# Kernel tuning notes

Measured on AMD Instinct MI355X. Metric: run time of the kernel, lower is better.

The kernel has to match this reference:

```python
import jax, jax.numpy as jnp
import numpy as np

B, S, D = 32, 2048, 1024
TEMP = 9.0  # RelaxedBernoulli temperature (torch.tensor([9]))


def setup_inputs() -> dict:
    key = jax.random.key(0)
    ks = jax.random.split(key, 12)
    sd = 1.0 / np.sqrt(D)
    sd2 = 1.0 / np.sqrt(2 * D)
    return {
        "h_t": jax.random.normal(ks[0], (B, D), jnp.float32),
        "h_s": jax.random.normal(ks[1], (B, S, D), jnp.float32),
        "auxi_hs": jax.random.normal(ks[2], (B, S, D), jnp.float32),
        "noise_u": jax.random.uniform(ks[3], (B, S, 1), jnp.float32),
        # linear_map: Linear(2*dim, 1) with bias
        "Wmap": jax.random.normal(ks[4], (2 * D,), jnp.float32) * sd2,
        "bmap": jax.random.normal(ks[5], (), jnp.float32) * sd2,
        # mlp_h: Linear(dim, dim) + Tanh + Linear(dim, 1)
        "W1": jax.random.normal(ks[6], (D, D), jnp.float32) * sd,
        "b1": jax.random.normal(ks[7], (D,), jnp.float32) * sd,
        "W2": jax.random.normal(ks[8], (D,), jnp.float32) * sd,
        "b2": jax.random.normal(ks[9], (), jnp.float32) * sd,
        # linear_out: Linear(2*dim, dim, bias=False) (attn_type='dot')
        "Wout": jax.random.normal(ks[10], (D, 2 * D), jnp.float32) * sd2,
    }


def reference(h_t, h_s, auxi_hs, noise_u, Wmap, bmap, W1, b1, W2, b2, Wout):
    # h_t: (B, D) one-step query; h_s, auxi_hs: (B, S, D)
    d = h_s.shape[-1]
    # linear_map(concat(auxi_hs, H_t)) without materializing the (B,S,2D) concat
    Wm_a, Wm_t = Wmap[:d], Wmap[d:]
    logits_p = jnp.einsum('bsd,d->bs', auxi_hs, Wm_a) + (h_t @ Wm_t)[:, None] + bmap  # (B,S)
    logits_p = logits_p[..., None]  # (B,S,1); note logit(sigmoid(x)) == x
    # RelaxedBernoulli(temp=9, probs=sigmoid(logits_p)).sample() with explicit uniform noise
    eps = 1e-7
    u = jnp.clip(noise_u, eps, 1.0 - eps)
    logistic = jnp.log(u) - jnp.log1p(-u)  # (B,S,1)
    G = jax.nn.sigmoid((logits_p + logistic) / TEMP)  # (B,S,1)
    # mlp_h(h_s): Linear -> tanh -> Linear
    e = jnp.einsum('bsd,d->bs', jnp.tanh(jnp.einsum('bsd,ed->bse', h_s, W1) + b1), W2) + b2
    e = e[..., None]  # (B,S,1)
    # custom softmax: max over dim 0 (batch!), exp, gate
    v = jnp.max(e, axis=0, keepdims=True)  # (1,S,1)
    scores = jnp.exp(e - v) * G  # (B,S,1)
    align = scores[..., 0] / jnp.sum(scores[..., 0], axis=1, keepdims=True)  # (B,S)
    c = jnp.einsum('bs,bsd->bd', align, h_s)  # (B,D)
    attn_h = jnp.tanh(jnp.concatenate([c, h_t], axis=-1) @ Wout.T)  # (B,D)
    return attn_h, align
```

## Files before the change

kernel.cpp:

```cpp
#include <hip/hip_runtime.h>
#include <hip/hip_bf16.h>
#include <math.h>

#define B_ 32
#define S_ 2048
#define D_ 1024
#define TEMP_ 9.0f

typedef __attribute__((ext_vector_type(8))) short short8;
typedef __attribute__((ext_vector_type(4))) float f32x4;
typedef __attribute__((ext_vector_type(4))) unsigned short ushort4v;

__device__ __forceinline__ unsigned short f2b(float f) {
  union { float f; unsigned int u; } v; v.f = f;
  unsigned int r = v.u;
  r += 0x7fffu + ((r >> 16) & 1u);
  return (unsigned short)(r >> 16);
}
__device__ __forceinline__ float b2f(unsigned short b) {
  union { float f; unsigned int u; } v; v.u = ((unsigned int)b) << 16;
  return v.f;
}
__device__ __forceinline__ float tanh_fast(float x) {
  float ez = __expf(2.f * x);
  return 1.f - __fdividef(2.f, ez + 1.f);
}

#define GLOAD_LDS16(g, l) \
  __builtin_amdgcn_global_load_lds((const __attribute__((address_space(1))) void*)(g), \
                                   (__attribute__((address_space(3))) void*)(l), 16, 0, 0)

__global__ void k_conv(const float* __restrict__ src, unsigned short* __restrict__ dst, int n8) {
  int i = blockIdx.x * 256 + threadIdx.x;
  if (i >= n8) return;
  const float4* g = reinterpret_cast<const float4*>(src) + (size_t)i * 2;
  float4 x0 = g[0], x1 = g[1];
  uint4 w;
  w.x = f2b(x0.x) | ((unsigned)f2b(x0.y) << 16);
  w.y = f2b(x0.z) | ((unsigned)f2b(x0.w) << 16);
  w.z = f2b(x1.x) | ((unsigned)f2b(x1.y) << 16);
  w.w = f2b(x1.z) | ((unsigned)f2b(x1.w) << 16);
  reinterpret_cast<uint4*>(dst)[i] = w;
}

__global__ void k0_tdot(const float* __restrict__ h_t, const float* __restrict__ Wmap,
                        const float* __restrict__ bmap, float* __restrict__ tdot) {
  int b = blockIdx.x;
  int t = threadIdx.x;
  float p = 0.f;
  for (int k = t; k < D_; k += 256) p += h_t[b*D_ + k] * Wmap[D_ + k];
  __shared__ float red[256];
  red[t] = p; __syncthreads();
  for (int off = 128; off > 0; off >>= 1) { if (t < off) red[t] += red[t+off]; __syncthreads(); }
  if (t == 0) tdot[b] = red[0] + bmap[0];
}

__global__ void k1_gate(const float* __restrict__ aux, const float* __restrict__ Wmap,
                        const float* __restrict__ noise, const float* __restrict__ tdot,
                        float* __restrict__ Gout) {
  int w = (blockIdx.x * 256 + threadIdx.x) >> 6;
  int lane = threadIdx.x & 63;
  const float4* arow = reinterpret_cast<const float4*>(aux + (size_t)w * D_);
  const float4* wrow = reinterpret_cast<const float4*>(Wmap);
  float p = 0.f;
  for (int it = 0; it < 4; ++it) {
    float4 a = arow[it*64 + lane];
    float4 m = wrow[it*64 + lane];
    p += a.x*m.x + a.y*m.y + a.z*m.z + a.w*m.w;
  }
  for (int msk = 32; msk > 0; msk >>= 1) p += __shfl_xor(p, msk);
  if (lane == 0) {
    int b = w >> 11;
    float logits = p + tdot[b];
    float u = noise[w];
    u = fminf(fmaxf(u, 1e-7f), 1.f - 1e-7f);
    float logistic = logf(u) - log1pf(-u);
    float x = (logits + logistic) / TEMP_;
    Gout[w] = 1.f / (1.f + expf(-x));
  }
}

#define BK3 32
#define NT3 (D_ / BK3)

extern __shared__ unsigned short lds2[];

__global__ __launch_bounds__(512, 2) void k2_pipe(
    const unsigned short* __restrict__ Ag, const unsigned short* __restrict__ Bg,
    const float* __restrict__ b1, const float* __restrict__ W2,
    float* __restrict__ e_buf) {
  int hw = blockIdx.x;
  int xcd = hw & 7;
  int sub = hw >> 3;
  int cc  = sub & 3;
  int rc  = xcd + 8 * (sub >> 2);
  int rowBase = rc * 256;
  int colBase = cc * 256;

  int t = threadIdx.x;
  int lane = t & 63;
  int wv = t >> 6;
  int wr = wv >> 2, wc = wv & 3;
  int kslot = lane >> 4;

  int aOff[8], bOff[4];
#pragma unroll
  for (int m = 0; m < 8; ++m) {
    int ra = wr * 128 + m * 16 + (lane & 15);
    aOff[m] = ra * 64 + ((kslot ^ ((ra >> 1) & 3)) << 4);
  }
#pragma unroll
  for (int n = 0; n < 4; ++n) {
    int rb = wc * 64 + n * 16 + (lane & 15);
    bOff[n] = 16384 + rb * 64 + ((kslot ^ ((rb >> 1) & 3)) << 4);
  }

  const unsigned short* gA[2];
  const unsigned short* gB[2];
  int dstOff[2];
#pragma unroll
  for (int i = 0; i < 2; ++i) {
    int c = i * 512 + t;
    int r = c >> 2;
    int clog = (c & 3) ^ ((r >> 1) & 3);
    gA[i] = Ag + (size_t)(rowBase + r) * D_ + clog * 8;
    gB[i] = Bg + (size_t)(colBase + r) * D_ + clog * 8;
    dstOff[i] = c * 16;
  }

  f32x4 acc[8][4] = {};

#define STAGE(TT) do {                                                         \
    char* _ba = (char*)lds2 + ((TT) & 3) * 32768;                              \
    GLOAD_LDS16(gA[0] + (TT) * 32, _ba + dstOff[0]);                           \
    GLOAD_LDS16(gA[1] + (TT) * 32, _ba + dstOff[1]);                           \
    GLOAD_LDS16(gB[0] + (TT) * 32, _ba + 16384 + dstOff[0]);                   \
    GLOAD_LDS16(gB[1] + (TT) * 32, _ba + 16384 + dstOff[1]);                   \
  } while (0)

#define K2_TILE(T, VM, DO_STAGE) do {                                          \
    asm volatile("s_waitcnt lgkmcnt(0)\n\ts_waitcnt vmcnt(" #VM ")" ::: "memory"); \
    __builtin_amdgcn_s_barrier();                                              \
    if (DO_STAGE) STAGE((T) + 3);                                              \
    const char* _ab = (const char*)lds2 + ((T) & 3) * 32768;                   \
    short8 af[8], bf[4];                                                       \
    _Pragma("unroll")                                                          \
    for (int n = 0; n < 4; ++n)                                                \
      bf[n] = *reinterpret_cast<const short8*>(_ab + bOff[n]);                 \
    _Pragma("unroll")                                                          \
    for (int m = 0; m < 4; ++m)                                                \
      af[m] = *reinterpret_cast<const short8*>(_ab + aOff[m]);                 \
    __builtin_amdgcn_s_setprio(1);                                             \
    _Pragma("unroll")                                                          \
    for (int m = 0; m < 4; ++m)                                                \
      _Pragma("unroll")                                                        \
      for (int n = 0; n < 4; ++n)                                              \
        acc[m][n] = __builtin_amdgcn_mfma_f32_16x16x32_bf16(af[m], bf[n], acc[m][n], 0, 0, 0); \
    _Pragma("unroll")                                                          \
    for (int m = 4; m < 8; ++m)                                                \
      af[m] = *reinterpret_cast<const short8*>(_ab + aOff[m]);                 \
    _Pragma("unroll")                                                          \
    for (int m = 4; m < 8; ++m)                                                \
      _Pragma("unroll")                                                        \
      for (int n = 0; n < 4; ++n)                                              \
        acc[m][n] = __builtin_amdgcn_mfma_f32_16x16x32_bf16(af[m], bf[n], acc[m][n], 0, 0, 0); \
    __builtin_amdgcn_s_setprio(0);                                             \
  } while (0)

  STAGE(0); STAGE(1); STAGE(2);
#pragma unroll
  for (int tt = 0; tt < 28; ++tt) K2_TILE(tt, 8, true);
  K2_TILE(28, 8, true);
  K2_TILE(29, 8, false);
  K2_TILE(30, 4, false);
  K2_TILE(31, 0, false);
#undef K2_TILE
#undef STAGE

  float b1v[4], w2v[4];
#pragma unroll
  for (int n = 0; n < 4; ++n) {
    int col = colBase + wc * 64 + n * 16 + (lane & 15);
    b1v[n] = b1[col];
    w2v[n] = W2[col];
  }
#pragma unroll
  for (int m = 0; m < 8; ++m) {
#pragma unroll
    for (int j = 0; j < 4; ++j) {
      float s = 0.f;
#pragma unroll
      for (int n = 0; n < 4; ++n)
        s += tanh_fast(acc[m][n][j] + b1v[n]) * w2v[n];
      s += __shfl_xor(s, 1);
      s += __shfl_xor(s, 2);
      s += __shfl_xor(s, 4);
      s += __shfl_xor(s, 8);
      if ((lane & 15) == 0) {
        int row = rowBase + wr * 128 + m * 16 + ((lane >> 4) << 2) + j;
        atomicAdd(&e_buf[row], s);
      }
    }
  }
}

#define BM 128
#define BN 128
#define BK 64
__global__ __launch_bounds__(256) void k2_egemm_f32(
    const float* __restrict__ h_s, const float* __restrict__ W1,
    const float* __restrict__ b1, const float* __restrict__ W2,
    float* __restrict__ e_buf) {
  __shared__ unsigned short As[BM * BK];
  __shared__ unsigned short Bs[BN * BK];
  int bid = blockIdx.x;
  int colBase = (bid & 7) * BN;
  int rowBase = (bid >> 3) * BM;
  int t = threadIdx.x;
  int lane = t & 63;
  int wave = t >> 6;
  int wr = wave >> 1, wc = wave & 1;
  f32x4 acc[4][4] = {};
  for (int k0 = 0; k0 < D_; k0 += BK) {
    __syncthreads();
    for (int i = 0; i < 4; ++i) {
      int flat = i*256 + t;
      int r = flat >> 3;
      int c8 = flat & 7;
      int byte = (r*128 + c8*16) ^ ((r & 7) << 4);
      {
        const float4* g = reinterpret_cast<const float4*>(h_s + (size_t)(rowBase + r)*D_ + k0 + c8*8);
        float4 x0 = g[0], x1 = g[1];
        uint4 w;
        w.x = f2b(x0.x) | ((unsigned)f2b(x0.y) << 16);
        w.y = f2b(x0.z) | ((unsigned)f2b(x0.w) << 16);
        w.z = f2b(x1.x) | ((unsigned)f2b(x1.y) << 16);
        w.w = f2b(x1.z) | ((unsigned)f2b(x1.w) << 16);
        *reinterpret_cast<uint4*>(reinterpret_cast<char*>(As) + byte) = w;
      }
      {
        const float4* g = reinterpret_cast<const float4*>(W1 + (size_t)(colBase + r)*D_ + k0 + c8*8);
        float4 x0 = g[0], x1 = g[1];
        uint4 w;
        w.x = f2b(x0.x) | ((unsigned)f2b(x0.y) << 16);
        w.y = f2b(x0.z) | ((unsigned)f2b(x0.w) << 16);
        w.z = f2b(x1.x) | ((unsigned)f2b(x1.y) << 16);
        w.w = f2b(x1.z) | ((unsigned)f2b(x1.w) << 16);
        *reinterpret_cast<uint4*>(reinterpret_cast<char*>(Bs) + byte) = w;
      }
    }
    __syncthreads();
    for (int kk = 0; kk < BK; kk += 32) {
      short8 af[4], bf[4];
      int kByte = kk*2 + ((lane >> 4) << 4);
      for (int m = 0; m < 4; ++m) {
        int r = wr*64 + m*16 + (lane & 15);
        int byte = (r*128 + kByte) ^ ((r & 7) << 4);
        af[m] = *reinterpret_cast<const short8*>(reinterpret_cast<const char*>(As) + byte);
      }
      for (int n = 0; n < 4; ++n) {
        int r = wc*64 + n*16 + (lane & 15);
        int byte = (r*128 + kByte) ^ ((r & 7) << 4);
        bf[n] = *reinterpret_cast<const short8*>(reinterpret_cast<const char*>(Bs) + byte);
      }
      for (int m = 0; m < 4; ++m)
        for (int n = 0; n < 4; ++n)
          acc[m][n] = __builtin_amdgcn_mfma_f32_16x16x32_bf16(af[m], bf[n], acc[m][n], 0, 0, 0);
    }
  }
  float b1v[4], w2v[4];
  for (int n = 0; n < 4; ++n) {
    int col = colBase + wc*64 + n*16 + (lane & 15);
    b1v[n] = b1[col];
    w2v[n] = W2[col];
  }
  for (int m = 0; m < 4; ++m) {
    for (int j = 0; j < 4; ++j) {
      float s = 0.f;
      for (int n = 0; n < 4; ++n)
        s += tanhf(acc[m][n][j] + b1v[n]) * w2v[n];
      s += __shfl_xor(s, 1);
      s += __shfl_xor(s, 2);
      s += __shfl_xor(s, 4);
      s += __shfl_xor(s, 8);
      if ((lane & 15) == 0) {
        int row = rowBase + wr*64 + m*16 + ((lane >> 4) << 2) + j;
        atomicAdd(&e_buf[row], s);
      }
    }
  }
}

__global__ void k3a_vmax(const float* __restrict__ e_buf, float* __restrict__ v) {
  int s = blockIdx.x * 256 + threadIdx.x;
  if (s >= S_) return;
  float m = -1e30f;
  for (int b = 0; b < B_; ++b) m = fmaxf(m, e_buf[b*S_ + s]);
  v[s] = m;
}

__global__ void k3b_align(const float* __restrict__ e_buf, const float* __restrict__ v,
                          float* __restrict__ galign) {
  int b = blockIdx.x;
  int t = threadIdx.x;
  __shared__ float sc[S_];
  __shared__ float red[256];
  float p = 0.f;
  for (int s = t; s < S_; s += 256) {
    float x = expf(e_buf[b*S_ + s] - v[s]) * galign[b*S_ + s];
    sc[s] = x;
    p += x;
  }
  red[t] = p; __syncthreads();
  for (int off = 128; off > 0; off >>= 1) { if (t < off) red[t] += red[t+off]; __syncthreads(); }
  float inv = 1.f / red[0];
  for (int s = t; s < S_; s += 256) galign[b*S_ + s] = sc[s] * inv;
}

__global__ void k4_ctx_bf16(const unsigned short* __restrict__ hsb, const float* __restrict__ align,
                            float* __restrict__ c) {
  int bid = blockIdx.x;
  int b = bid >> 6;
  int sBase = (bid & 63) * 32;
  int t = threadIdx.x;
  float4 accv = {0.f, 0.f, 0.f, 0.f};
  for (int si = 0; si < 32; ++si) {
    int s = sBase + si;
    float a = align[b*S_ + s];
    ushort4v hv = *reinterpret_cast<const ushort4v*>(hsb + (size_t)(b*S_ + s)*D_ + t*4);
    accv.x += a*b2f(hv.x); accv.y += a*b2f(hv.y); accv.z += a*b2f(hv.z); accv.w += a*b2f(hv.w);
  }
  atomicAdd(&c[b*D_ + t*4 + 0], accv.x);
  atomicAdd(&c[b*D_ + t*4 + 1], accv.y);
  atomicAdd(&c[b*D_ + t*4 + 2], accv.z);
  atomicAdd(&c[b*D_ + t*4 + 3], accv.w);
}

__global__ void k4_ctx_f32(const float* __restrict__ h_s, const float* __restrict__ align,
                           float* __restrict__ c) {
  int bid = blockIdx.x;
  int b = bid >> 6;
  int sBase = (bid & 63) * 32;
  int t = threadIdx.x;
  float4 accv = {0.f, 0.f, 0.f, 0.f};
  for (int si = 0; si < 32; ++si) {
    int s = sBase + si;
    float a = align[b*S_ + s];
    float4 hv = *reinterpret_cast<const float4*>(h_s + (size_t)(b*S_ + s)*D_ + t*4);
    accv.x += a*hv.x; accv.y += a*hv.y; accv.z += a*hv.z; accv.w += a*hv.w;
  }
  atomicAdd(&c[b*D_ + t*4 + 0], accv.x);
  atomicAdd(&c[b*D_ + t*4 + 1], accv.y);
  atomicAdd(&c[b*D_ + t*4 + 2], accv.z);
  atomicAdd(&c[b*D_ + t*4 + 3], accv.w);
}

__global__ void k5_out(const float* __restrict__ c, const float* __restrict__ h_t,
                       const float* __restrict__ Wout, float* __restrict__ out) {
  int W = (blockIdx.x * 256 + threadIdx.x) >> 6;
  int lane = threadIdx.x & 63;
  int b = W >> 10;
  int o = W & 1023;
  const float* wrow = Wout + (size_t)o * (2 * D_);
  float p = 0.f;
  for (int it = 0; it < 16; ++it) {
    int k = it*64 + lane;
    p += c[b*D_ + k] * wrow[k];
  }
  for (int it = 16; it < 32; ++it) {
    int k = it*64 + lane;
    p += h_t[b*D_ + (k - D_)] * wrow[k];
  }
  for (int m = 32; m > 0; m >>= 1) p += __shfl_xor(p, m);
  if (lane == 0) out[b*D_ + o] = tanhf(p);
}

extern "C" void kernel_launch(void* const* d_in, const int* in_sizes, int n_in,
                              void* d_out, int out_size, void* d_ws, size_t ws_size,
                              hipStream_t stream) {
  const float* h_t   = (const float*)d_in[0];
  const float* h_s   = (const float*)d_in[1];
  const float* aux   = (const float*)d_in[2];
  const float* noise = (const float*)d_in[3];
  const float* Wmap  = (const float*)d_in[4];
  const float* bmap  = (const float*)d_in[5];
  const float* W1    = (const float*)d_in[6];
  const float* b1    = (const float*)d_in[7];
  const float* W2    = (const float*)d_in[8];
  const float* Wout  = (const float*)d_in[10];

  float* out    = (float*)d_out;
  float* galign = out + B_*D_;

  const size_t HS_N   = (size_t)B_*S_*D_;
  const size_t W1_N   = (size_t)D_*D_;
  const size_t needed = HS_N*2 + W1_N*2 + (65536 + 32 + 2048 + 32768) * sizeof(float);

  if (ws_size >= needed) {
    unsigned short* hs_bf = (unsigned short*)d_ws;
    unsigned short* w1_bf = hs_bf + HS_N;
    float* fws   = (float*)(w1_bf + W1_N);
    float* e_buf = fws;
    float* tdot  = fws + 65536;
    float* v     = fws + 65568;
    float* c     = fws + 67616;

    hipMemsetAsync(e_buf, 0, 65536 * sizeof(float), stream);
    hipMemsetAsync(c, 0, 32768 * sizeof(float), stream);

    hipFuncSetAttribute(reinterpret_cast<const void*>(k2_pipe),
                        hipFuncAttributeMaxDynamicSharedMemorySize, 131072);

    k_conv<<<(int)(HS_N/8/256), 256, 0, stream>>>(h_s, hs_bf, (int)(HS_N/8));
    k_conv<<<(int)(W1_N/8/256), 256, 0, stream>>>(W1, w1_bf, (int)(W1_N/8));
    k0_tdot<<<32, 256, 0, stream>>>(h_t, Wmap, bmap, tdot);
    k1_gate<<<16384, 256, 0, stream>>>(aux, Wmap, noise, tdot, galign);
    k2_pipe<<<1024, 512, 131072, stream>>>(hs_bf, w1_bf, b1, W2, e_buf);
    k3a_vmax<<<8, 256, 0, stream>>>(e_buf, v);
    k3b_align<<<32, 256, 0, stream>>>(e_buf, v, galign);
    k4_ctx_bf16<<<2048, 256, 0, stream>>>(hs_bf, galign, c);
    k5_out<<<8192, 256, 0, stream>>>(c, h_t, Wout, out);
  } else {
    float* ws    = (float*)d_ws;
    float* e_buf = ws;
    float* tdot  = ws + 65536;
    float* v     = ws + 65568;
    float* c     = ws + 67616;

    hipMemsetAsync(e_buf, 0, 65536 * sizeof(float), stream);
    hipMemsetAsync(c, 0, 32768 * sizeof(float), stream);

    k0_tdot<<<32, 256, 0, stream>>>(h_t, Wmap, bmap, tdot);
    k1_gate<<<16384, 256, 0, stream>>>(aux, Wmap, noise, tdot, galign);
    k2_egemm_f32<<<4096, 256, 0, stream>>>(h_s, W1, b1, W2, e_buf);
    k3a_vmax<<<8, 256, 0, stream>>>(e_buf, v);
    k3b_align<<<32, 256, 0, stream>>>(e_buf, v, galign);
    k4_ctx_f32<<<2048, 256, 0, stream>>>(h_s, galign, c);
    k5_out<<<8192, 256, 0, stream>>>(c, h_t, Wout, out);
  }
}
```

Baseline: 362.3 us.

## Load GEMM B fragments directly from global into registers, halve LDS staging

The bf16 GEMM kernel no longer stages the W1 (B) tile through LDS. Each wave now loads its B fragments straight from global memory into registers, double-buffered one k-tile ahead, so LDS only holds the A ring and the dynamic shared memory drops from 128KB to 64KB. This removes LDS write/read traffic for B and the lgkmcnt wait, and may let more blocks fit per CU. The cost is more global loads, since the B tile is now fetched per wave rather than once per block, plus extra register pressure and retuned vmcnt counts that must stay correct.

Result: slower. 435.6 us (+20.2%).

```diff
diff --git a/kernel.cpp b/kernel.cpp
--- a/kernel.cpp
+++ b/kernel.cpp
@@ -103,50 +103,53 @@
   int wr = wv >> 2, wc = wv & 3;
   int kslot = lane >> 4;
 
-  int aOff[8], bOff[4];
+  int aOff[8];
 #pragma unroll
   for (int m = 0; m < 8; ++m) {
     int ra = wr * 128 + m * 16 + (lane & 15);
     aOff[m] = ra * 64 + ((kslot ^ ((ra >> 1) & 3)) << 4);
   }
+
+  const unsigned short* gA[2];
+  int dstOff0, dstOff1;
+  {
+    int c0 = t, c1 = 512 + t;
+    int r0 = c0 >> 2, r1 = c1 >> 2;
+    int cl0 = (c0 & 3) ^ ((r0 >> 1) & 3);
+    int cl1 = (c1 & 3) ^ ((r1 >> 1) & 3);
+    gA[0] = Ag + (size_t)(rowBase + r0) * D_ + cl0 * 8;
+    gA[1] = Ag + (size_t)(rowBase + r1) * D_ + cl1 * 8;
+    dstOff0 = c0 * 16;
+    dstOff1 = c1 * 16;
+  }
+
+  const unsigned short* gBf[4];
 #pragma unroll
   for (int n = 0; n < 4; ++n) {
-    int rb = wc * 64 + n * 16 + (lane & 15);
-    bOff[n] = 16384 + rb * 64 + ((kslot ^ ((rb >> 1) & 3)) << 4);
-  }
-
-  const unsigned short* gA[2];
-  const unsigned short* gB[2];
-  int dstOff[2];
-#pragma unroll
-  for (int i = 0; i < 2; ++i) {
-    int c = i * 512 + t;
-    int r = c >> 2;
-    int clog = (c & 3) ^ ((r >> 1) & 3);
-    gA[i] = Ag + (size_t)(rowBase + r) * D_ + clog * 8;
-    gB[i] = Bg + (size_t)(colBase + r) * D_ + clog * 8;
-    dstOff[i] = c * 16;
+    int col = colBase + wc * 64 + n * 16 + (lane & 15);
+    gBf[n] = Bg + (size_t)col * D_ + kslot * 8;
   }
 
   f32x4 acc[8][4] = {};
-
-#define STAGE(TT) do {                                                         \
-    char* _ba = (char*)lds2 + ((TT) & 3) * 32768;                              \
-    GLOAD_LDS16(gA[0] + (TT) * 32, _ba + dstOff[0]);                           \
-    GLOAD_LDS16(gA[1] + (TT) * 32, _ba + dstOff[1]);                           \
-    GLOAD_LDS16(gB[0] + (TT) * 32, _ba + 16384 + dstOff[0]);                   \
-    GLOAD_LDS16(gB[1] + (TT) * 32, _ba + 16384 + dstOff[1]);                   \
+  short8 bfA[4], bfB[4];
+
+#define STAGE_A(TT) do {                                                       \
+    char* _ba = (char*)lds2 + ((TT) & 3) * 16384;                              \
+    GLOAD_LDS16(gA[0] + (TT) * 32, _ba + dstOff0);                             \
+    GLOAD_LDS16(gA[1] + (TT) * 32, _ba + dstOff1);                             \
   } while (0)
 
-#define K2_TILE(T, VM, DO_STAGE) do {                                          \
-    asm volatile("s_waitcnt lgkmcnt(0)\n\ts_waitcnt vmcnt(" #VM ")" ::: "memory"); \
+#define K2_TILE(T, VM, DO_STAGE, DO_B, BFC, BFN) do {                          \
+    asm volatile("s_waitcnt vmcnt(" #VM ")" ::: "memory");                     \
     __builtin_amdgcn_s_barrier();                                              \
-    if (DO_STAGE) STAGE((T) + 3);                                              \
-    const char* _ab = (const char*)lds2 + ((T) & 3) * 32768;                   \
-    short8 af[8], bf[4];                                                       \
-    _Pragma("unroll")                                                          \
-    for (int n = 0; n < 4; ++n)                                                \
-      bf[n] = *reinterpret_cast<const short8*>(_ab + bOff[n]);                 \
+    if (DO_B) {                                                                \
+      _Pragma("unroll")                                                        \
+      for (int n = 0; n < 4; ++n)                                              \
+        BFN[n] = *reinterpret_cast<const short8*>(gBf[n] + ((T) + 1) * 32);    \
+    }                                                                          \
+    if (DO_STAGE) STAGE_A((T) + 3);                                            \
+    const char* _ab = (const char*)lds2 + ((T) & 3) * 16384;                   \
+    short8 af[8];                                                              \
     _Pragma("unroll")                                                          \
     for (int m = 0; m < 4; ++m)                                                \
       af[m] = *reinterpret_cast<const short8*>(_ab + aOff[m]);                 \
@@ -155,27 +158,38 @@
     for (int m = 0; m < 4; ++m)                                                \
       _Pragma("unroll")                                                        \
       for (int n = 0; n < 4; ++n)                                              \
-        acc[m][n] = __builtin_amdgcn_mfma_f32_16x16x32_bf16(af[m], bf[n], acc[m][n], 0, 0, 0); \
+        acc[m][n] = __builtin_amdgcn_mfma_f32_16x16x32_bf16(af[m], BFC[n], acc[m][n], 0, 0, 0); \
+    __builtin_amdgcn_s_setprio(0);                                             \
     _Pragma("unroll")                                                          \
     for (int m = 4; m < 8; ++m)                                                \
       af[m] = *reinterpret_cast<const short8*>(_ab + aOff[m]);                 \
+    __builtin_amdgcn_s_setprio(1);                                             \
     _Pragma("unroll")                                                          \
     for (int m = 4; m < 8; ++m)                                                \
       _Pragma("unroll")                                                        \
       for (int n = 0; n < 4; ++n)                                              \
-        acc[m][n] = __builtin_amdgcn_mfma_f32_16x16x32_bf16(af[m], bf[n], acc[m][n], 0, 0, 0); \
+        acc[m][n] = __builtin_amdgcn_mfma_f32_16x16x32_bf16(af[m], BFC[n], acc[m][n], 0, 0, 0); \
     __builtin_amdgcn_s_setprio(0);                                             \
   } while (0)
 
-  STAGE(0); STAGE(1); STAGE(2);
-#pragma unroll
-  for (int tt = 0; tt < 28; ++tt) K2_TILE(tt, 8, true);
-  K2_TILE(28, 8, true);
-  K2_TILE(29, 8, false);
-  K2_TILE(30, 4, false);
-  K2_TILE(31, 0, false);
+#pragma unroll
+  for (int n = 0; n < 4; ++n)
+    bfA[n] = *reinterpret_cast<const short8*>(gBf[n]);
+  STAGE_A(0); STAGE_A(1); STAGE_A(2);
+
+  K2_TILE(0, 4, true, true, bfA, bfB);
+  K2_TILE(1, 8, true, true, bfB, bfA);
+#pragma unroll
+  for (int tt = 2; tt < 28; tt += 2) {
+    K2_TILE(tt,     12, true, true, bfA, bfB);
+    K2_TILE(tt + 1, 12, true, true, bfB, bfA);
+  }
+  K2_TILE(28, 12, true,  true,  bfA, bfB);
+  K2_TILE(29, 12, false, true,  bfB, bfA);
+  K2_TILE(30, 10, false, true,  bfA, bfB);
+  K2_TILE(31, 8,  false, false, bfB, bfA);
 #undef K2_TILE
-#undef STAGE
+#undef STAGE_A
 
   float b1v[4], w2v[4];
 #pragma unroll
@@ -409,13 +423,13 @@
     hipMemsetAsync(c, 0, 32768 * sizeof(float), stream);
 
     hipFuncSetAttribute(reinterpret_cast<const void*>(k2_pipe),
-                        hipFuncAttributeMaxDynamicSharedMemorySize, 131072);
+                        hipFuncAttributeMaxDynamicSharedMemorySize, 65536);
 
     k_conv<<<(int)(HS_N/8/256), 256, 0, stream>>>(h_s, hs_bf, (int)(HS_N/8));
     k_conv<<<(int)(W1_N/8/256), 256, 0, stream>>>(W1, w1_bf, (int)(W1_N/8));
     k0_tdot<<<32, 256, 0, stream>>>(h_t, Wmap, bmap, tdot);
     k1_gate<<<16384, 256, 0, stream>>>(aux, Wmap, noise, tdot, galign);
-    k2_pipe<<<1024, 512, 131072, stream>>>(hs_bf, w1_bf, b1, W2, e_buf);
+    k2_pipe<<<1024, 512, 65536, stream>>>(hs_bf, w1_bf, b1, W2, e_buf);
     k3a_vmax<<<8, 256, 0, stream>>>(e_buf, v);
     k3b_align<<<32, 256, 0, stream>>>(e_buf, v, galign);
     k4_ctx_bf16<<<2048, 256, 0, stream>>>(hs_bf, galign, c);
```

## Shrink GEMM block tile to 128x256 with 4 waves and triple buffering

Applied to the files above, without the earlier changes.

The bf16 MLP GEMM kernel moves from 256x256 tiles with 8 waves and 4 LDS buffers to 128x256 tiles with 4 waves and 3 LDS buffers (72KB), launching twice as many blocks. The next-tile prefetch is issued after the first LDS fragment reads rather than before them, and priority is dropped around the second batch of A reads. The aim is lower LDS use per block so more blocks fit per CU, plus better load/compute interleaving. The cost is less B-tile reuse per block, which doubles global traffic for W1, and a shallower prefetch distance.

Result: no change. 357.2 us (-1.4%).

```diff
diff --git a/kernel.cpp b/kernel.cpp
--- a/kernel.cpp
+++ b/kernel.cpp
@@ -82,10 +82,14 @@
 
 #define BK3 32
 #define NT3 (D_ / BK3)
+#define A_BYTES 8192
+#define B_BYTES 16384
+#define BUF_BYTES 24576
+#define NBUF 3
 
 extern __shared__ unsigned short lds2[];
 
-__global__ __launch_bounds__(512, 2) void k2_pipe(
+__global__ __launch_bounds__(256, 2) void k2_pipe(
     const unsigned short* __restrict__ Ag, const unsigned short* __restrict__ Bg,
     const float* __restrict__ b1, const float* __restrict__ W2,
     float* __restrict__ e_buf) {
@@ -94,55 +98,62 @@
   int sub = hw >> 3;
   int cc  = sub & 3;
   int rc  = xcd + 8 * (sub >> 2);
-  int rowBase = rc * 256;
+  int rowBase = rc * 128;
   int colBase = cc * 256;
 
   int t = threadIdx.x;
   int lane = t & 63;
-  int wv = t >> 6;
-  int wr = wv >> 2, wc = wv & 3;
+  int wc = t >> 6;
   int kslot = lane >> 4;
 
   int aOff[8], bOff[4];
 #pragma unroll
   for (int m = 0; m < 8; ++m) {
-    int ra = wr * 128 + m * 16 + (lane & 15);
+    int ra = m * 16 + (lane & 15);
     aOff[m] = ra * 64 + ((kslot ^ ((ra >> 1) & 3)) << 4);
   }
 #pragma unroll
   for (int n = 0; n < 4; ++n) {
     int rb = wc * 64 + n * 16 + (lane & 15);
-    bOff[n] = 16384 + rb * 64 + ((kslot ^ ((rb >> 1) & 3)) << 4);
+    bOff[n] = A_BYTES + rb * 64 + ((kslot ^ ((rb >> 1) & 3)) << 4);
   }
 
   const unsigned short* gA[2];
-  const unsigned short* gB[2];
-  int dstOff[2];
+  const unsigned short* gB[4];
+  int dstA[2], dstB[4];
 #pragma unroll
   for (int i = 0; i < 2; ++i) {
-    int c = i * 512 + t;
+    int c = i * 256 + t;
     int r = c >> 2;
     int clog = (c & 3) ^ ((r >> 1) & 3);
     gA[i] = Ag + (size_t)(rowBase + r) * D_ + clog * 8;
+    dstA[i] = c * 16;
+  }
+#pragma unroll
+  for (int i = 0; i < 4; ++i) {
+    int c = i * 256 + t;
+    int r = c >> 2;
+    int clog = (c & 3) ^ ((r >> 1) & 3);
     gB[i] = Bg + (size_t)(colBase + r) * D_ + clog * 8;
-    dstOff[i] = c * 16;
+    dstB[i] = A_BYTES + c * 16;
   }
 
   f32x4 acc[8][4] = {};
 
 #define STAGE(TT) do {                                                         \
-    char* _ba = (char*)lds2 + ((TT) & 3) * 32768;                              \
-    GLOAD_LDS16(gA[0] + (TT) * 32, _ba + dstOff[0]);                           \
-    GLOAD_LDS16(gA[1] + (TT) * 32, _ba + dstOff[1]);                           \
-    GLOAD_LDS16(gB[0] + (TT) * 32, _ba + 16384 + dstOff[0]);                   \
-    GLOAD_LDS16(gB[1] + (TT) * 32, _ba + 16384 + dstOff[1]);                   \
+    char* _ba = (char*)lds2 + ((TT) % NBUF) * BUF_BYTES;                       \
+    GLOAD_LDS16(gA[0] + (TT) * 32, _ba + dstA[0]);                             \
+    GLOAD_LDS16(gA[1] + (TT) * 32, _ba + dstA[1]);                             \
+    GLOAD_LDS16(gB[0] + (TT) * 32, _ba + dstB[0]);                             \
+    GLOAD_LDS16(gB[1] + (TT) * 32, _ba + dstB[1]);                             \
+    GLOAD_LDS16(gB[2] + (TT) * 32, _ba + dstB[2]);                             \
+    GLOAD_LDS16(gB[3] + (TT) * 32, _ba + dstB[3]);                             \
   } while (0)
 
 #define K2_TILE(T, VM, DO_STAGE) do {                                          \
     asm volatile("s_waitcnt lgkmcnt(0)\n\ts_waitcnt vmcnt(" #VM ")" ::: "memory"); \
     __builtin_amdgcn_s_barrier();                                              \
-    if (DO_STAGE) STAGE((T) + 3);                                              \
-    const char* _ab = (const char*)lds2 + ((T) & 3) * 32768;                   \
+    const char* _ab = (const char*)lds2 + ((T) % NBUF) * BUF_BYTES;            \
     short8 af[8], bf[4];                                                       \
     _Pragma("unroll")                                                          \
     for (int n = 0; n < 4; ++n)                                                \
@@ -150,15 +161,18 @@
     _Pragma("unroll")                                                          \
     for (int m = 0; m < 4; ++m)                                                \
       af[m] = *reinterpret_cast<const short8*>(_ab + aOff[m]);                 \
+    if (DO_STAGE) STAGE((T) + 2);                                              \
     __builtin_amdgcn_s_setprio(1);                                             \
     _Pragma("unroll")                                                          \
     for (int m = 0; m < 4; ++m)                                                \
       _Pragma("unroll")                                                        \
       for (int n = 0; n < 4; ++n)                                              \
         acc[m][n] = __builtin_amdgcn_mfma_f32_16x16x32_bf16(af[m], bf[n], acc[m][n], 0, 0, 0); \
+    __builtin_amdgcn_s_setprio(0);                                             \
     _Pragma("unroll")                                                          \
     for (int m = 4; m < 8; ++m)                                                \
       af[m] = *reinterpret_cast<const short8*>(_ab + aOff[m]);                 \
+    __builtin_amdgcn_s_setprio(1);                                             \
     _Pragma("unroll")                                                          \
     for (int m = 4; m < 8; ++m)                                                \
       _Pragma("unroll")                                                        \
@@ -167,12 +181,10 @@
     __builtin_amdgcn_s_setprio(0);                                             \
   } while (0)
 
-  STAGE(0); STAGE(1); STAGE(2);
-#pragma unroll
-  for (int tt = 0; tt < 28; ++tt) K2_TILE(tt, 8, true);
-  K2_TILE(28, 8, true);
-  K2_TILE(29, 8, false);
-  K2_TILE(30, 4, false);
+  STAGE(0); STAGE(1);
+#pragma unroll
+  for (int tt = 0; tt < 30; ++tt) K2_TILE(tt, 6, true);
+  K2_TILE(30, 6, false);
   K2_TILE(31, 0, false);
 #undef K2_TILE
 #undef STAGE
@@ -197,7 +209,7 @@
       s += __shfl_xor(s, 4);
       s += __shfl_xor(s, 8);
       if ((lane & 15) == 0) {
-        int row = rowBase + wr * 128 + m * 16 + ((lane >> 4) << 2) + j;
+        int row = rowBase + m * 16 + ((lane >> 4) << 2) + j;
         atomicAdd(&e_buf[row], s);
       }
     }
@@ -409,13 +421,13 @@
     hipMemsetAsync(c, 0, 32768 * sizeof(float), stream);
 
     hipFuncSetAttribute(reinterpret_cast<const void*>(k2_pipe),
-                        hipFuncAttributeMaxDynamicSharedMemorySize, 131072);
+                        hipFuncAttributeMaxDynamicSharedMemorySize, NBUF * BUF_BYTES);
 
     k_conv<<<(int)(HS_N/8/256), 256, 0, stream>>>(h_s, hs_bf, (int)(HS_N/8));
     k_conv<<<(int)(W1_N/8/256), 256, 0, stream>>>(W1, w1_bf, (int)(W1_N/8));
     k0_tdot<<<32, 256, 0, stream>>>(h_t, Wmap, bmap, tdot);
     k1_gate<<<16384, 256, 0, stream>>>(aux, Wmap, noise, tdot, galign);
-    k2_pipe<<<1024, 512, 131072, stream>>>(hs_bf, w1_bf, b1, W2, e_buf);
+    k2_pipe<<<2048, 256, NBUF * BUF_BYTES, stream>>>(hs_bf, w1_bf, b1, W2, e_buf);
     k3a_vmax<<<8, 256, 0, stream>>>(e_buf, v);
     k3b_align<<<32, 256, 0, stream>>>(e_buf, v, galign);
     k4_ctx_bf16<<<2048, 256, 0, stream>>>(hs_bf, galign, c);
```
